# Performance work log

Hardware: AMD Instinct MI355X
Metric: run time of the kernel (lower is better)

Reference implementation:

```python
import jax, jax.numpy as jnp
import numpy as np
from jax import lax

DN = ('NCHW', 'OIHW', 'NCHW')


def setup_inputs() -> dict:
    key = jax.random.key(0)
    ks = jax.random.split(key, 4)
    b, C, H, W = 8, 512, 64, 64
    heads = 8
    return {
        'x': jax.random.normal(ks[0], (b, C, H, W), jnp.float32),
        'qkv_w': jax.random.normal(ks[1], (3 * C, C, 1, 1), jnp.float32) * 0.02,
        'dw_w': jax.random.normal(ks[2], (3 * C, 1, 3, 3), jnp.float32) * 0.02,
        'proj_w': jax.random.normal(ks[3], (C, C, 1, 1), jnp.float32) * 0.02,
        'temperature': jnp.ones((heads, 1, 1), jnp.float32),
        'a1': jnp.full((1,), 0.2, jnp.float32),
        'a2': jnp.full((1,), 0.2, jnp.float32),
        'a3': jnp.full((1,), 0.2, jnp.float32),
        'a4': jnp.full((1,), 0.2, jnp.float32),
    }


def _masked_softmax(attn, k):
    # keep top-k entries per row (same set as torch topk+scatter mask for
    # generic floats), -inf elsewhere, then stable softmax
    thr = lax.top_k(attn, k)[0][..., -1:]
    return jax.nn.softmax(jnp.where(attn >= thr, attn, -jnp.inf), axis=-1)


def _l2norm(t):
    return t / jnp.maximum(jnp.linalg.norm(t, axis=-1, keepdims=True), 1e-12)


def reference(x, qkv_w, dw_w, proj_w, temperature, a1, a2, a3, a4):
    b, c, h, w = x.shape
    heads = temperature.shape[0]
    # 1x1 pointwise conv then 3x3 depthwise conv (groups = 3c)
    qkv = lax.conv_general_dilated(x, qkv_w, (1, 1), 'SAME', dimension_numbers=DN)
    qkv = lax.conv_general_dilated(qkv, dw_w, (1, 1), 'SAME',
                                   feature_group_count=3 * c, dimension_numbers=DN)
    q, k, v = jnp.split(qkv, 3, axis=1)
    # b (head Cph) h w -> b head Cph (h w)
    resh = lambda t: t.reshape(b, heads, c // heads, h * w)
    q, k, v = resh(q), resh(k), resh(v)
    q = _l2norm(q)
    k = _l2norm(k)
    C = q.shape[2]  # channels per head = 64
    attn = jnp.einsum('bhcn,bhdn->bhcd', q, k) * temperature  # (b,heads,C,C)
    out = (_masked_softmax(attn, C // 2) @ v) * a1 \
        + (_masked_softmax(attn, (C * 2) // 3) @ v) * a2 \
        + (_masked_softmax(attn, (C * 3) // 4) @ v) * a3 \
        + (_masked_softmax(attn, (C * 4) // 5) @ v) * a4
    out = out.reshape(b, c, h, w)
    out = lax.conv_general_dilated(out, proj_w, (1, 1), 'SAME', dimension_numbers=DN)
    return out
```

## Files before the change

kernel.cpp:

```cpp
#include <hip/hip_runtime.h>
#include <hip/hip_bf16.h>

#define CHN 512
#define HW  4096
#define C3  1536
#define GB  4

typedef __hip_bfloat16 bf16;
typedef __attribute__((ext_vector_type(8))) short short8;
typedef __attribute__((ext_vector_type(4))) short short4v;
typedef __attribute__((ext_vector_type(4))) float f32x4;
typedef __attribute__((ext_vector_type(4))) int   int4v;
typedef _Float16 h8_t __attribute__((ext_vector_type(8)));

__device__ inline float b2f_bits(short s) {
    union { unsigned u; float f; } uf;
    uf.u = ((unsigned)(unsigned short)s) << 16;
    return uf.f;
}
__device__ inline short f2b_bits(float x) {
    union { __hip_bfloat16 h; short s; } u;
    u.h = __float2bfloat16(x);
    return u.s;
}
__device__ inline void split_bf16(float x, short& hi, short& lo) {
    hi = f2b_bits(x);
    lo = f2b_bits(x - b2f_bits(hi));
}
__device__ inline int pack_split(float x) {
    short h, l;
    split_bf16(x, h, l);
    return (int)((unsigned short)h | ((unsigned)(unsigned short)l << 16));
}
__device__ inline short f2h_bits(float x) {
    _Float16 h = (_Float16)x;
    return __builtin_bit_cast(short, h);
}
__device__ inline float h2f_bits(short s) {
    return (float)__builtin_bit_cast(_Float16, s);
}
__device__ inline int swz64(int row, int g) {
    return row * 64 + ((g ^ (row & 7)) << 3);
}
__device__ inline int swz128(int row, int g) {
    return row * 128 + ((g ^ (row & 15)) << 3);
}
__device__ inline void gload16(const void* g, void* l) {
    __builtin_amdgcn_global_load_lds(
        (const __attribute__((address_space(1))) void*)g,
        (__attribute__((address_space(3))) void*)l, 16, 0, 0);
}

__global__ __launch_bounds__(256) void k_w_hi(const float* __restrict__ w,
                                              short* __restrict__ wh, int n4) {
    int i = blockIdx.x * 256 + threadIdx.x;
    if (i < n4) {
        f32x4 v = *(const f32x4*)&w[i * 4];
        short4v h;
#pragma unroll
    for (int j = 0; j < 4; ++j) h[j] = f2h_bits(v[j]);
        *(short4v*)&wh[i * 4] = h;
    }
}

__global__ __launch_bounds__(256) void k_transpose_xf16(const float* __restrict__ in,
                                                        short* __restrict__ out) {
    __shared__ float tile[64][65];
    int b = blockIdx.z;
    int c0 = blockIdx.y * 64, n0 = blockIdx.x * 64;
    const float* ip = in + (long)b * ((long)CHN * HW);
    short* op = out + (long)b * ((long)HW * CHN);
    int t = threadIdx.x;
#pragma unroll
    for (int p = 0; p < 4; ++p) {
        int id = p * 256 + t;
        int r = id >> 4, c4 = (id & 15) * 4;
        f32x4 v = *(const f32x4*)&ip[(long)(c0 + r) * HW + n0 + c4];
#pragma unroll
        for (int j = 0; j < 4; ++j) tile[r][c4 + j] = v[j];
    }
    __syncthreads();
    int col = t & 63, rr = t >> 6;
#pragma unroll
    for (int p = 0; p < 16; ++p) {
        int r = p * 4 + rr;
        op[(long)(n0 + r) * CHN + c0 + col] = f2h_bits(tile[col][r]);
    }
}

template <int MT, bool OUT_F16>
__global__ __launch_bounds__(256) void k_gemm_f16(const short* __restrict__ Ah,
                                                  const short* __restrict__ B,
                                                  void* __restrict__ Cv,
                                                  int M, int N, int K,
                                                  long bB, long bC, long rstride) {
    __shared__ short sAh[MT * 64], sB[128 * 64];
    int b = blockIdx.z;
    int m0 = blockIdx.y * MT, n0 = blockIdx.x * 128;
    const short* Bp = B + (long)b * bB;
    int t = threadIdx.x, wid = t >> 6, lane = t & 63;
    int wr = (wid >> 1) * (MT / 2), wc = (wid & 1) * 64;
    int lrow = lane & 15, khalf = lane >> 4;
    int lrow8 = lane >> 3;
    int gl = ((lane & 7) ^ lrow8) << 3;
    constexpr int MR = MT / 32;
    f32x4 acc[MR][4] = {};
    for (int kt = 0; kt < K; kt += 64) {
#pragma unroll
        for (int i = 0; i < MT / 32; ++i) {
            int rb = i * 32 + wid * 8;
            int row = rb + lrow8;
            gload16(&Ah[(long)(m0 + row) * K + kt + gl], &sAh[rb * 64]);
        }
#pragma unroll
        for (int i = 0; i < 4; ++i) {
            int rb = i * 32 + wid * 8;
            int row = rb + lrow8;
            gload16(&Bp[(long)(n0 + row) * K + kt + gl], &sB[rb * 64]);
        }
        __syncthreads();
#pragma unroll
        for (int ks = 0; ks < 2; ++ks) {
            int gk = ks * 4 + khalf;
            h8_t ah[MR], bh[4];
#pragma unroll
            for (int i = 0; i < MR; ++i)
                ah[i] = *(const h8_t*)&sAh[swz64(wr + i * 16 + lrow, gk)];
#pragma unroll
            for (int i = 0; i < 4; ++i)
                bh[i] = *(const h8_t*)&sB[swz64(wc + i * 16 + lrow, gk)];
#pragma unroll
            for (int mi = 0; mi < MR; ++mi)
#pragma unroll
                for (int ni = 0; ni < 4; ++ni)
                    acc[mi][ni] = __builtin_amdgcn_mfma_f32_16x16x32_f16(
                        ah[mi], bh[ni], acc[mi][ni], 0, 0, 0);
        }
        __syncthreads();
    }
    int crow = (lane >> 4) * 4, ccol = lane & 15;
#pragma unroll
    for (int mi = 0; mi < MR; ++mi)
#pragma unroll
        for (int ni = 0; ni < 4; ++ni)
#pragma unroll
            for (int r = 0; r < 4; ++r) {
                long row = m0 + wr + mi * 16 + crow + r;
                long col = n0 + wc + ni * 16 + ccol;
                float v = acc[mi][ni][r];
                if constexpr (OUT_F16)
                    ((short*)Cv)[(long)b * bC + row * rstride + col] = f2h_bits(v);
                else
                    ((float*)Cv)[(long)b * bC + row * rstride + col] = v;
            }
}

__global__ __launch_bounds__(256) void k_dwl2_rs(int* __restrict__ qkv,
                                                 const float* __restrict__ w) {
    __shared__ float red[4];
    int ch = blockIdx.x, b = blockIdx.y;
    bool is_qk = ch < 1024;
    int* pi = qkv + ((long)b * C3 + ch) * HW;
    short* ps = (short*)pi;
    const short* pin = (const short*)pi;
    float w9[9];
#pragma unroll
    for (int i = 0; i < 9; ++i) w9[i] = w[ch * 9 + i];
    int t = threadIdx.x, wid = t >> 6, lane = t & 63;
    int y0 = wid * 16;
    float out[16];
#pragma unroll
    for (int j = 0; j < 16; ++j) out[j] = 0.f;
#pragma unroll
    for (int i = 0; i < 18; ++i) {
        int r = y0 - 1 + i;
        float v = (r >= 0 && r < 64) ? h2f_bits(pin[r * 64 + lane]) : 0.f;
        float vl = __shfl_up(v, 1);
        float vr = __shfl_down(v, 1);
        if (lane == 0) vl = 0.f;
        if (lane == 63) vr = 0.f;
        int j = i - 1;
        if (j + 1 >= 0 && j + 1 < 16) out[j + 1] += w9[0] * vl + w9[1] * v + w9[2] * vr;
        if (j >= 0 && j < 16)         out[j]     += w9[3] * vl + w9[4] * v + w9[5] * vr;
        if (j - 1 >= 0 && j - 1 < 16) out[j - 1] += w9[6] * vl + w9[7] * v + w9[8] * vr;
    }
    if (is_qk) {
        float ss = 0.f;
#pragma unroll
        for (int j = 0; j < 16; ++j) ss += out[j] * out[j];
#pragma unroll
        for (int o = 32; o; o >>= 1) ss += __shfl_xor(ss, o);
        if (lane == 0) red[wid] = ss;
        __syncthreads();
        float tot = red[0] + red[1] + red[2] + red[3];
        float sc = 1.f / fmaxf(sqrtf(tot), 1e-12f);
#pragma unroll
        for (int j = 0; j < 16; ++j) {
            short hi, lo;
            split_bf16(out[j] * sc, hi, lo);
            int n = (y0 + j) * 64 + lane;
            ps[n] = hi;
            ps[4096 + n] = lo;
        }
    } else {
        __syncthreads();
#pragma unroll
        for (int j = 0; j < 16; ++j)
            pi[(y0 + j) * 64 + lane] = pack_split(out[j]);
    }
}

__global__ __launch_bounds__(256) void k_attn_gl(const short* __restrict__ qkv_sh,
                                                 float* __restrict__ attn_part) {
    __shared__ short sQh[64 * 128], sQl[64 * 128], sKh[64 * 128], sKl[64 * 128];
    int h = blockIdx.x, ksl = blockIdx.y, b = blockIdx.z;
    const short* qb = qkv_sh + ((long)b * C3 + h * 64) * (HW * 2L);
    const short* kb = qb + (long)512 * HW * 2;
    int t = threadIdx.x, wid = t >> 6, lane = t & 63;
    int lrow = lane & 15, khalf = lane >> 4;
    f32x4 acc[4] = {};
    for (int kt = ksl * 512; kt < ksl * 512 + 512; kt += 128) {
#pragma unroll
        for (int i = 0; i < 4; ++i) {
            int rb = wid * 16 + i * 4;
            int row = rb + (lane >> 4);
            int gsrc = ((lane & 15) ^ (row & 15)) << 3;
            const short* qrow = qb + (long)row * (HW * 2L) + kt + gsrc;
            const short* krow = kb + (long)row * (HW * 2L) + kt + gsrc;
            gload16(qrow,        &sQh[rb * 128]);
            gload16(qrow + 4096, &sQl[rb * 128]);
            gload16(krow,        &sKh[rb * 128]);
            gload16(krow + 4096, &sKl[rb * 128]);
        }
        __syncthreads();
#pragma unroll
        for (int ks = 0; ks < 4; ++ks) {
            int gk = ks * 4 + khalf;
            short8 kh = *(const short8*)&sKh[swz128(wid * 16 + lrow, gk)];
            short8 kl = *(const short8*)&sKl[swz128(wid * 16 + lrow, gk)];
#pragma unroll
            for (int mi = 0; mi < 4; ++mi) {
                short8 qh = *(const short8*)&sQh[swz128(mi * 16 + lrow, gk)];
                short8 ql = *(const short8*)&sQl[swz128(mi * 16 + lrow, gk)];
                acc[mi] = __builtin_amdgcn_mfma_f32_16x16x32_bf16(qh, kh, acc[mi], 0, 0, 0);
                acc[mi] = __builtin_amdgcn_mfma_f32_16x16x32_bf16(ql, kh, acc[mi], 0, 0, 0);
                acc[mi] = __builtin_amdgcn_mfma_f32_16x16x32_bf16(qh, kl, acc[mi], 0, 0, 0);
            }
        }
        __syncthreads();
    }
    float* op = attn_part + (((long)b * 8 + ksl) * 8 + h) * 4096;
    int crow = (lane >> 4) * 4, ccol = lane & 15;
#pragma unroll
    for (int mi = 0; mi < 4; ++mi)
#pragma unroll
        for (int r = 0; r < 4; ++r)
            op[(mi * 16 + crow + r) * 64 + wid * 16 + ccol] = acc[mi][r];
}

__global__ __launch_bounds__(256) void k_smcomb(const float* __restrict__ attn_part,
                                                const float* __restrict__ temp,
                                                const float* __restrict__ a1,
                                                const float* __restrict__ a2,
                                                const float* __restrict__ a3,
                                                const float* __restrict__ a4,
                                                float* __restrict__ Wc) {
    int t = threadIdx.x, wid = t >> 6, lane = t & 63;
    int b = blockIdx.z;
    int r = blockIdx.x * 4 + wid;
    int h = r >> 6, qr = r & 63;
    float a = 0.f;
#pragma unroll
    for (int s = 0; s < 8; ++s)
        a += attn_part[(((long)b * 8 + s) * 8 + h) * 4096 + qr * 64 + lane];
    a *= temp[h];
    int cnt = 0;
#pragma unroll
    for (int j = 0; j < 64; ++j) {
        float aj = __shfl(a, j);
        cnt += (aj > a) ? 1 : 0;
    }
    float m = a;
#pragma unroll
    for (int o = 32; o; o >>= 1) m = fmaxf(m, __shfl_xor(m, o));
    float e = expf(a - m);
    const int kk[4] = {32, 42, 48, 51};
    float coef[4] = {a1[0], a2[0], a3[0], a4[0]};
    float out = 0.f;
#pragma unroll
    for (int i = 0; i < 4; ++i) {
        float ei = (cnt < kk[i]) ? e : 0.f;
        float d = ei;
#pragma unroll
        for (int o = 32; o; o >>= 1) d += __shfl_xor(d, o);
        out += coef[i] * ei / d;
    }
    Wc[((long)b * 8 + h) * 4096 + qr * 64 + lane] = out;
}

__global__ __launch_bounds__(256) void k_wv_pp(const float* __restrict__ Wc,
                                               const int* __restrict__ qkv_pp,
                                               short* __restrict__ attTs) {
    __shared__ int sVi[64 * 128];
    __shared__ short sWh[64 * 64], sWl[64 * 64];
    int nb = blockIdx.x, h = blockIdx.y, b = blockIdx.z;
    int n0 = nb * 128;
    const float* wp = Wc + ((long)b * 8 + h) * 4096;
    const int* vp = qkv_pp + ((long)b * C3 + 1024 + h * 64) * HW;
    int t = threadIdx.x, wid = t >> 6, lane = t & 63;
    int lrow = lane & 15, khalf = lane >> 4;
#pragma unroll
    for (int p = 0; p < 8; ++p) {
        int id = p * 256 + t;
        int d = id >> 5, c4 = (id & 31) * 4;
        int4v v = *(const int4v*)&vp[(long)d * HW + n0 + c4];
        int cs = c4 ^ (((d >> 3) & 3) << 3);
        *(int4v*)&sVi[d * 128 + cs] = v;
    }
#pragma unroll
    for (int p = 0; p < 2; ++p) {
        int id = p * 256 + t, row = id >> 3, g = id & 7;
        f32x4 va = *(const f32x4*)&wp[row * 64 + g * 8];
        f32x4 vb = *(const f32x4*)&wp[row * 64 + g * 8 + 4];
        short8 hh, ll;
#pragma unroll
        for (int j = 0; j < 4; ++j) {
            short h0, l0, h1, l1;
            split_bf16(va[j], h0, l0);
            split_bf16(vb[j], h1, l1);
            hh[j] = h0;     ll[j] = l0;
            hh[4 + j] = h1; ll[4 + j] = l1;
        }
        int off = swz64(row, g);
        *(short8*)&sWh[off] = hh;
        *(short8*)&sWl[off] = ll;
    }
    __syncthreads();
    f32x4 acc[2][4] = {};
#pragma unroll
    for (int ks = 0; ks < 2; ++ks) {
        int gk = ks * 4 + khalf;
        short8 vh[2], vl[2], wh[4], wl[4];
#pragma unroll
        for (int i = 0; i < 2; ++i) {
            int nrow = wid * 32 + i * 16 + lrow;
            int col = nrow ^ ((gk & 3) << 3);
            int vi[8];
#pragma unroll
            for (int j = 0; j < 8; ++j)
                vi[j] = sVi[(gk * 8 + j) * 128 + col];
            int hi_[4], lo_[4];
#pragma unroll
            for (int m = 0; m < 4; ++m) {
                unsigned a = (unsigned)vi[2 * m], c = (unsigned)vi[2 * m + 1];
                hi_[m] = (int)((a & 0xffffu) | (c << 16));
                lo_[m] = (int)((a >> 16) | (c & 0xffff0000u));
            }
            int4v hv = {hi_[0], hi_[1], hi_[2], hi_[3]};
            int4v lv = {lo_[0], lo_[1], lo_[2], lo_[3]};
            vh[i] = __builtin_bit_cast(short8, hv);
            vl[i] = __builtin_bit_cast(short8, lv);
        }
#pragma unroll
        for (int i = 0; i < 4; ++i) {
            int rr = i * 16 + lrow;
            wh[i] = *(const short8*)&sWh[swz64(rr, gk)];
            wl[i] = *(const short8*)&sWl[swz64(rr, gk)];
        }
#pragma unroll
        for (int mi = 0; mi < 2; ++mi)
#pragma unroll
            for (int ni = 0; ni < 4; ++ni) {
                acc[mi][ni] = __builtin_amdgcn_mfma_f32_16x16x32_bf16(
                    vh[mi], wh[ni], acc[mi][ni], 0, 0, 0);
                acc[mi][ni] = __builtin_amdgcn_mfma_f32_16x16x32_bf16(
                    vl[mi], wh[ni], acc[mi][ni], 0, 0, 0);
                acc[mi][ni] = __builtin_amdgcn_mfma_f32_16x16x32_bf16(
                    vh[mi], wl[ni], acc[mi][ni], 0, 0, 0);
            }
    }
    short* op = attTs + (long)b * ((long)C3 * HW * 2);
    int crow = (lane >> 4) * 4, ccol = lane & 15;
#pragma unroll
    for (int mi = 0; mi < 2; ++mi)
#pragma unroll
        for (int ni = 0; ni < 4; ++ni)
#pragma unroll
            for (int r = 0; r < 4; ++r) {
                long n = n0 + wid * 32 + mi * 16 + crow + r;
                int c = h * 64 + ni * 16 + ccol;
                op[n * CHN + c] = f2h_bits(acc[mi][ni][r]);
            }
}

extern "C" void kernel_launch(void* const* d_in, const int* in_sizes, int n_in,
                              void* d_out, int out_size, void* d_ws, size_t ws_size,
                              hipStream_t stream) {
    const float* x      = (const float*)d_in[0];
    const float* qkv_w  = (const float*)d_in[1];
    const float* dw_w   = (const float*)d_in[2];
    const float* proj_w = (const float*)d_in[3];
    const float* temp   = (const float*)d_in[4];
    const float* a1     = (const float*)d_in[5];
    const float* a2     = (const float*)d_in[6];
    const float* a3     = (const float*)d_in[7];
    const float* a4     = (const float*)d_in[8];
    float* out = (float*)d_out;

    char* ws = (char*)d_ws;
    int*   qkvi      = (int*)(ws);
    short* xTs       = (short*)(ws + 100663296);
    short* wqh       = (short*)(ws + 134217728);
    float* attn_part = (float*)(ws + 134217728);
    float* Wc        = (float*)(ws + 138412032);
    short* wph       = (short*)(ws + 138936320);

    k_w_hi<<<256, 256, 0, stream>>>(proj_w, wph, 65536);

    for (int g = 0; g < 2; ++g) {
        const float* xg = x + (long)g * GB * CHN * HW;
        float* outg = out + (long)g * GB * CHN * HW;
        k_w_hi<<<768, 256, 0, stream>>>(qkv_w, wqh, 196608);
        k_transpose_xf16<<<dim3(64, 8, GB), 256, 0, stream>>>(xg, xTs);
        k_gemm_f16<128, true><<<dim3(32, 12, GB), 256, 0, stream>>>(
            wqh, xTs, qkvi, C3, HW, CHN,
            (long)HW * CHN, (long)C3 * 8192, 8192);
        k_dwl2_rs<<<dim3(C3, GB), 256, 0, stream>>>(qkvi, dw_w);
        k_attn_gl<<<dim3(8, 8, GB), 256, 0, stream>>>((const short*)qkvi, attn_part);
        k_smcomb<<<dim3(128, 1, GB), 256, 0, stream>>>(attn_part, temp, a1, a2, a3, a4, Wc);
        k_wv_pp<<<dim3(32, 8, GB), 256, 0, stream>>>(Wc, qkvi, (short*)qkvi);
        k_gemm_f16<64, false><<<dim3(32, 8, GB), 256, 0, stream>>>(
            wph, (const short*)qkvi, outg, CHN, HW, CHN,
            (long)C3 * HW * 2, (long)CHN * HW, HW);
    }
}
```

Before: 273.3 us.

## Store V as single fp16, stage GEMM epilogue through LDS, hoist weight conversion

The V channels are now written as plain fp16 instead of packed bf16 hi/lo pairs. The weighted-V kernel therefore loads half the data, skips the unpacking shuffles, and runs two fp16 MFMAs per tile instead of three bf16 ones, keeping a hi/lo split only on the softmax weights. The f16-output GEMM epilogue now stages results through swizzled LDS so it can issue vectorized row stores instead of scattered 2-byte writes. The qkv weight conversion moves out of the per-group loop into its own workspace slot. V now carries fp16 precision only, which costs some accuracy.

```diff
diff --git a/kernel.cpp b/kernel.cpp
--- a/kernel.cpp
+++ b/kernel.cpp
@@ -27,17 +27,18 @@
     hi = f2b_bits(x);
     lo = f2b_bits(x - b2f_bits(hi));
 }
-__device__ inline int pack_split(float x) {
-    short h, l;
-    split_bf16(x, h, l);
-    return (int)((unsigned short)h | ((unsigned)(unsigned short)l << 16));
-}
 __device__ inline short f2h_bits(float x) {
     _Float16 h = (_Float16)x;
     return __builtin_bit_cast(short, h);
 }
 __device__ inline float h2f_bits(short s) {
     return (float)__builtin_bit_cast(_Float16, s);
+}
+__device__ inline void split_f16(float x, short& hi, short& lo) {
+    _Float16 h = (_Float16)x;
+    _Float16 l = (_Float16)(x - (float)h);
+    hi = __builtin_bit_cast(short, h);
+    lo = __builtin_bit_cast(short, l);
 }
 __device__ inline int swz64(int row, int g) {
     return row * 64 + ((g ^ (row & 7)) << 3);
@@ -58,7 +59,7 @@
         f32x4 v = *(const f32x4*)&w[i * 4];
         short4v h;
 #pragma unroll
-    for (int j = 0; j < 4; ++j) h[j] = f2h_bits(v[j]);
+        for (int j = 0; j < 4; ++j) h[j] = f2h_bits(v[j]);
         *(short4v*)&wh[i * 4] = h;
     }
 }
@@ -94,7 +95,9 @@
                                                   void* __restrict__ Cv,
                                                   int M, int N, int K,
                                                   long bB, long bC, long rstride) {
-    __shared__ short sAh[MT * 64], sB[128 * 64];
+    __shared__ short smem[(MT + 128) * 64];
+    short* sAh = smem;
+    short* sB  = smem + MT * 64;
     int b = blockIdx.z;
     int m0 = blockIdx.y * MT, n0 = blockIdx.x * 128;
     const short* Bp = B + (long)b * bB;
@@ -139,20 +142,41 @@
         __syncthreads();
     }
     int crow = (lane >> 4) * 4, ccol = lane & 15;
-#pragma unroll
-    for (int mi = 0; mi < MR; ++mi)
-#pragma unroll
-        for (int ni = 0; ni < 4; ++ni)
-#pragma unroll
-            for (int r = 0; r < 4; ++r) {
-                long row = m0 + wr + mi * 16 + crow + r;
-                long col = n0 + wc + ni * 16 + ccol;
-                float v = acc[mi][ni][r];
-                if constexpr (OUT_F16)
-                    ((short*)Cv)[(long)b * bC + row * rstride + col] = f2h_bits(v);
-                else
-                    ((float*)Cv)[(long)b * bC + row * rstride + col] = v;
-            }
+    if constexpr (OUT_F16) {
+        short* rp = smem + wid * 4096;
+#pragma unroll
+        for (int mi = 0; mi < MR; ++mi)
+#pragma unroll
+            for (int ni = 0; ni < 4; ++ni)
+#pragma unroll
+                for (int r = 0; r < 4; ++r) {
+                    int row = mi * 16 + crow + r;
+                    int col = ni * 16 + ccol;
+                    int addr = row * 64 + ((((col >> 2) ^ (row & 15)) << 2) | (col & 3));
+                    rp[addr] = f2h_bits(acc[mi][ni][r]);
+                }
+        __syncthreads();
+        short* Cp = (short*)Cv + (long)b * bC + (long)(m0 + wr) * rstride + n0 + wc;
+#pragma unroll
+        for (int it = 0; it < 16; ++it) {
+            int row = it * 4 + (lane >> 4);
+            int c4 = lane & 15;
+            int addr = row * 64 + ((c4 ^ (row & 15)) << 2);
+            short4v v4 = *(short4v*)&rp[addr];
+            *(short4v*)&Cp[(long)row * rstride + c4 * 4] = v4;
+        }
+    } else {
+#pragma unroll
+        for (int mi = 0; mi < MR; ++mi)
+#pragma unroll
+            for (int ni = 0; ni < 4; ++ni)
+#pragma unroll
+                for (int r = 0; r < 4; ++r) {
+                    long row = m0 + wr + mi * 16 + crow + r;
+                    long col = n0 + wc + ni * 16 + ccol;
+                    ((float*)Cv)[(long)b * bC + row * rstride + col] = acc[mi][ni][r];
+                }
+    }
 }
 
 __global__ __launch_bounds__(256) void k_dwl2_rs(int* __restrict__ qkv,
@@ -206,7 +230,7 @@
         __syncthreads();
 #pragma unroll
         for (int j = 0; j < 16; ++j)
-            pi[(y0 + j) * 64 + lane] = pack_split(out[j]);
+            ps[(y0 + j) * 64 + lane] = f2h_bits(out[j]);
     }
 }
 
@@ -298,24 +322,27 @@
     Wc[((long)b * 8 + h) * 4096 + qr * 64 + lane] = out;
 }
 
-__global__ __launch_bounds__(256) void k_wv_pp(const float* __restrict__ Wc,
-                                               const int* __restrict__ qkv_pp,
-                                               short* __restrict__ attTs) {
-    __shared__ int sVi[64 * 128];
+__global__ __launch_bounds__(256) void k_wv_f16(const float* __restrict__ Wc,
+                                                const short* __restrict__ qkv_sh,
+                                                short* __restrict__ attTs) {
+    __shared__ short sVt[128 * 64];
     __shared__ short sWh[64 * 64], sWl[64 * 64];
     int nb = blockIdx.x, h = blockIdx.y, b = blockIdx.z;
     int n0 = nb * 128;
     const float* wp = Wc + ((long)b * 8 + h) * 4096;
-    const int* vp = qkv_pp + ((long)b * C3 + 1024 + h * 64) * HW;
+    const short* vp = qkv_sh + ((long)b * C3 + 1024 + h * 64) * 8192L;
     int t = threadIdx.x, wid = t >> 6, lane = t & 63;
     int lrow = lane & 15, khalf = lane >> 4;
 #pragma unroll
-    for (int p = 0; p < 8; ++p) {
-        int id = p * 256 + t;
-        int d = id >> 5, c4 = (id & 31) * 4;
-        int4v v = *(const int4v*)&vp[(long)d * HW + n0 + c4];
-        int cs = c4 ^ (((d >> 3) & 3) << 3);
-        *(int4v*)&sVi[d * 128 + cs] = v;
+    for (int p = 0; p < 4; ++p) {
+        int d = lane;
+        int n8 = (p * 4 + wid) * 8;
+        short8 v8 = *(const short8*)&vp[(long)d * 8192 + n0 + n8];
+#pragma unroll
+        for (int j = 0; j < 8; ++j) {
+            int n = n8 + j;
+            sVt[n * 64 + (((d >> 3) ^ (n & 7)) << 3) + (d & 7)] = v8[j];
+        }
     }
 #pragma unroll
     for (int p = 0; p < 2; ++p) {
@@ -326,8 +353,8 @@
 #pragma unroll
         for (int j = 0; j < 4; ++j) {
             short h0, l0, h1, l1;
-            split_bf16(va[j], h0, l0);
-            split_bf16(vb[j], h1, l1);
+            split_f16(va[j], h0, l0);
+            split_f16(vb[j], h1, l1);
             hh[j] = h0;     ll[j] = l0;
             hh[4 + j] = h1; ll[4 + j] = l1;
         }
@@ -340,43 +367,26 @@
 #pragma unroll
     for (int ks = 0; ks < 2; ++ks) {
         int gk = ks * 4 + khalf;
-        short8 vh[2], vl[2], wh[4], wl[4];
+        h8_t vf[2], wh[4], wl[4];
 #pragma unroll
         for (int i = 0; i < 2; ++i) {
-            int nrow = wid * 32 + i * 16 + lrow;
-            int col = nrow ^ ((gk & 3) << 3);
-            int vi[8];
-#pragma unroll
-            for (int j = 0; j < 8; ++j)
-                vi[j] = sVi[(gk * 8 + j) * 128 + col];
-            int hi_[4], lo_[4];
-#pragma unroll
-            for (int m = 0; m < 4; ++m) {
-                unsigned a = (unsigned)vi[2 * m], c = (unsigned)vi[2 * m + 1];
-                hi_[m] = (int)((a & 0xffffu) | (c << 16));
-                lo_[m] = (int)((a >> 16) | (c & 0xffff0000u));
-            }
-            int4v hv = {hi_[0], hi_[1], hi_[2], hi_[3]};
-            int4v lv = {lo_[0], lo_[1], lo_[2], lo_[3]};
-            vh[i] = __builtin_bit_cast(short8, hv);
-            vl[i] = __builtin_bit_cast(short8, lv);
+            int n = wid * 32 + i * 16 + lrow;
+            vf[i] = *(const h8_t*)&sVt[n * 64 + ((gk ^ (n & 7)) << 3)];
         }
 #pragma unroll
         for (int i = 0; i < 4; ++i) {
             int rr = i * 16 + lrow;
-            wh[i] = *(const short8*)&sWh[swz64(rr, gk)];
-            wl[i] = *(const short8*)&sWl[swz64(rr, gk)];
+            wh[i] = *(const h8_t*)&sWh[swz64(rr, gk)];
+            wl[i] = *(const h8_t*)&sWl[swz64(rr, gk)];
         }
 #pragma unroll
         for (int mi = 0; mi < 2; ++mi)
 #pragma unroll
             for (int ni = 0; ni < 4; ++ni) {
-                acc[mi][ni] = __builtin_amdgcn_mfma_f32_16x16x32_bf16(
-                    vh[mi], wh[ni], acc[mi][ni], 0, 0, 0);
-                acc[mi][ni] = __builtin_amdgcn_mfma_f32_16x16x32_bf16(
-                    vl[mi], wh[ni], acc[mi][ni], 0, 0, 0);
-                acc[mi][ni] = __builtin_amdgcn_mfma_f32_16x16x32_bf16(
-                    vh[mi], wl[ni], acc[mi][ni], 0, 0, 0);
+                acc[mi][ni] = __builtin_amdgcn_mfma_f32_16x16x32_f16(
+                    vf[mi], wh[ni], acc[mi][ni], 0, 0, 0);
+                acc[mi][ni] = __builtin_amdgcn_mfma_f32_16x16x32_f16(
+                    vf[mi], wl[ni], acc[mi][ni], 0, 0, 0);
             }
     }
     short* op = attTs + (long)b * ((long)C3 * HW * 2);
@@ -410,17 +420,17 @@
     char* ws = (char*)d_ws;
     int*   qkvi      = (int*)(ws);
     short* xTs       = (short*)(ws + 100663296);
-    short* wqh       = (short*)(ws + 134217728);
     float* attn_part = (float*)(ws + 134217728);
     float* Wc        = (float*)(ws + 138412032);
     short* wph       = (short*)(ws + 138936320);
+    short* wqh       = (short*)(ws + 139460608);
 
     k_w_hi<<<256, 256, 0, stream>>>(proj_w, wph, 65536);
+    k_w_hi<<<768, 256, 0, stream>>>(qkv_w, wqh, 196608);
 
     for (int g = 0; g < 2; ++g) {
         const float* xg = x + (long)g * GB * CHN * HW;
         float* outg = out + (long)g * GB * CHN * HW;
-        k_w_hi<<<768, 256, 0, stream>>>(qkv_w, wqh, 196608);
         k_transpose_xf16<<<dim3(64, 8, GB), 256, 0, stream>>>(xg, xTs);
         k_gemm_f16<128, true><<<dim3(32, 12, GB), 256, 0, stream>>>(
             wqh, xTs, qkvi, C3, HW, CHN,
@@ -428,7 +438,7 @@
         k_dwl2_rs<<<dim3(C3, GB), 256, 0, stream>>>(qkvi, dw_w);
         k_attn_gl<<<dim3(8, 8, GB), 256, 0, stream>>>((const short*)qkvi, attn_part);
         k_smcomb<<<dim3(128, 1, GB), 256, 0, stream>>>(attn_part, temp, a1, a2, a3, a4, Wc);
-        k_wv_pp<<<dim3(32, 8, GB), 256, 0, stream>>>(Wc, qkvi, (short*)qkvi);
+        k_wv_f16<<<dim3(32, 8, GB), 256, 0, stream>>>(Wc, (const short*)qkvi, (short*)qkvi);
         k_gemm_f16<64, false><<<dim3(32, 8, GB), 256, 0, stream>>>(
             wph, (const short*)qkvi, outg, CHN, HW, CHN,
             (long)C3 * HW * 2, (long)CHN * HW, HW);
```

New measurement: 266.7 us. 1.02x faster.
